# Performance work log

Hardware: AMD Instinct MI355X
Metric: run time of the kernel (lower is better)

The kernel has to match this reference:

```python
import jax, jax.numpy as jnp
import numpy as np

VOCAB = 100000
DIM = 128
B = 262144
NEG = 5

def setup_inputs() -> dict:
    key = jax.random.key(0)
    k1, k2, k3, k4 = jax.random.split(key, 4)
    bound = 0.5 / DIM
    input_emb = jax.random.uniform(k4, (VOCAB, DIM), jnp.float32, -bound, bound)
    # original inits output embeddings to zeros; use small random so scores are nontrivial
    output_emb = jax.random.normal(jax.random.fold_in(key, 7), (VOCAB, DIM), jnp.float32) * 0.01
    target_words = jax.random.randint(k1, (B,), 0, VOCAB)
    context_words = jax.random.randint(k2, (B,), 0, VOCAB)
    negative_words = jax.random.randint(k3, (B, NEG), 0, VOCAB)
    return {"target_words": target_words, "context_words": context_words,
            "negative_words": negative_words, "input_emb": input_emb,
            "output_emb": output_emb}

def reference(target_words, context_words, negative_words, input_emb, output_emb):
    t = input_emb[target_words]               # [B, D]
    c = output_emb[context_words]             # [B, D]
    pos_scores = jnp.einsum('bd,bd->b', t, c) # [B]
    positive_loss = -jnp.mean(jax.nn.log_sigmoid(pos_scores))
    n = output_emb[negative_words]            # [B, NEG, D]
    neg_scores = jnp.einsum('bd,bnd->bn', t, n)  # [B, NEG]
    negative_loss = -jnp.mean(jax.nn.log_sigmoid(-neg_scores))
    return (positive_loss, negative_loss)
```

## Files before the change

kernel.cpp:

```cpp
#include <hip/hip_runtime.h>

#define VOCAB 100000
#define DIM 128
#define BATCH 262144
#define NEG 5

__device__ __forceinline__ float softplus_fast(float x) {
    return fmaxf(x, 0.0f) + __logf(1.0f + __expf(-fabsf(x)));
}

__device__ __forceinline__ float dot4(const float4 a, const float4 b) {
    return a.x * b.x + a.y * b.y + a.z * b.z + a.w * b.w;
}

__global__ void ns_init_kernel(float* acc) {
    acc[0] = 0.0f;
    acc[1] = 0.0f;
}

__global__ __launch_bounds__(256) void ns_loss_kernel(
    const int* __restrict__ tgt,
    const int* __restrict__ ctx,
    const int* __restrict__ negw,
    const float* __restrict__ iemb,
    const float* __restrict__ oemb,
    float* __restrict__ acc)
{
    const int tid = threadIdx.x;
    const int r   = tid & 7;
    const int grp = tid >> 3;
    const int e0  = blockIdx.x * 32 + grp;
    const int estride = gridDim.x * 32;

    float pos_acc = 0.0f, neg_acc = 0.0f;

    for (int e = e0; e < BATCH; e += estride) {
        const int tw = tgt[e];
        const int cw = ctx[e];

        const float4* tp = reinterpret_cast<const float4*>(iemb + (size_t)tw * DIM) + r * 4;
        const float4 t0 = tp[0], t1 = tp[1], t2 = tp[2], t3 = tp[3];

        const float4* cp = reinterpret_cast<const float4*>(oemb + (size_t)cw * DIM) + r * 4;
        float dp = dot4(t0, cp[0]) + dot4(t1, cp[1]) + dot4(t2, cp[2]) + dot4(t3, cp[3]);

        float dn[NEG];
        #pragma unroll
        for (int j = 0; j < NEG; ++j) {
            const int nw = negw[e * NEG + j];
            const float4* np_ = reinterpret_cast<const float4*>(oemb + (size_t)nw * DIM) + r * 4;
            dn[j] = dot4(t0, np_[0]) + dot4(t1, np_[1]) + dot4(t2, np_[2]) + dot4(t3, np_[3]);
        }

        #pragma unroll
        for (int m = 4; m >= 1; m >>= 1) {
            dp += __shfl_xor(dp, m, 64);
            #pragma unroll
            for (int j = 0; j < NEG; ++j) dn[j] += __shfl_xor(dn[j], m, 64);
        }

        pos_acc += softplus_fast(-dp);
        float s = 0.0f;
        #pragma unroll
        for (int j = 0; j < NEG; ++j) s += softplus_fast(dn[j]);
        neg_acc += s;
    }

    __shared__ float sp[256];
    __shared__ float sn[256];
    sp[tid] = pos_acc;
    sn[tid] = neg_acc;
    __syncthreads();
    #pragma unroll
    for (int s = 128; s > 0; s >>= 1) {
        if (tid < s) {
            sp[tid] += sp[tid + s];
            sn[tid] += sn[tid + s];
        }
        __syncthreads();
    }
    if (tid == 0) {
        atomicAdd(&acc[0], sp[0]);
        atomicAdd(&acc[1], sn[0]);
    }
}

__global__ void ns_finalize_kernel(const float* __restrict__ acc, float* __restrict__ out) {
    out[0] = acc[0] * (1.0f / ((float)BATCH * 8.0f));
    out[1] = acc[1] * (1.0f / ((float)BATCH * (float)NEG * 8.0f));
}

extern "C" void kernel_launch(void* const* d_in, const int* in_sizes, int n_in,
                              void* d_out, int out_size, void* d_ws, size_t ws_size,
                              hipStream_t stream) {
    const int*   tgt  = (const int*)d_in[0];
    const int*   ctx  = (const int*)d_in[1];
    const int*   negw = (const int*)d_in[2];
    const float* iemb = (const float*)d_in[3];
    const float* oemb = (const float*)d_in[4];
    float* out = (float*)d_out;
    float* acc = (float*)d_ws;

    ns_init_kernel<<<1, 1, 0, stream>>>(acc);
    ns_loss_kernel<<<2048, 256, 0, stream>>>(tgt, ctx, negw, iemb, oemb, acc);
    ns_finalize_kernel<<<1, 1, 0, stream>>>(acc, out);
}
```

Measured before the change: 151.8 us.

## Double-buffer embedding gathers into LDS with async global_load_lds and prefetched indices

Remaps work so each wave handles two batch elements per step with 32 lanes per row, and gathers all seven embedding rows straight into LDS through async global-to-LDS loads. The LDS buffers are double-buffered and indices are prefetched two iterations ahead, so memory latency overlaps with the dot products. The block-level LDS reduction is replaced by a wave shuffle and per-wave atomics, and the finalize scaling is updated for the 32-lane replication. This adds a dependency on the global_load_lds lane layout and a full vmcnt wait each iteration.

Result: slower. 278.1 us (+83.3%).

```diff
diff --git a/kernel.cpp b/kernel.cpp
--- a/kernel.cpp
+++ b/kernel.cpp
@@ -5,12 +5,26 @@
 #define BATCH 262144
 #define NEG 5
 
+#define NBLOCK 2048
+#define NTHREADS 256
+#define WAVES_PER_BLOCK 4
+#define NWAVES (NBLOCK * WAVES_PER_BLOCK)
+#define NPAIRS (BATCH / 2)
+#define NIT (NPAIRS / NWAVES)
+
 __device__ __forceinline__ float softplus_fast(float x) {
     return fmaxf(x, 0.0f) + __logf(1.0f + __expf(-fabsf(x)));
 }
 
-__device__ __forceinline__ float dot4(const float4 a, const float4 b) {
+__device__ __forceinline__ float dot4(float4 a, float4 b) {
     return a.x * b.x + a.y * b.y + a.z * b.z + a.w * b.w;
+}
+
+__device__ __forceinline__ void async_row16(const float* gsrc, float* ldst) {
+    __builtin_amdgcn_global_load_lds(
+        (const __attribute__((address_space(1))) void*)gsrc,
+        (__attribute__((address_space(3))) void*)ldst,
+        16, 0, 0);
 }
 
 __global__ void ns_init_kernel(float* acc) {
@@ -18,7 +32,7 @@
     acc[1] = 0.0f;
 }
 
-__global__ __launch_bounds__(256) void ns_loss_kernel(
+__global__ __launch_bounds__(NTHREADS) void ns_loss_kernel(
     const int* __restrict__ tgt,
     const int* __restrict__ ctx,
     const int* __restrict__ negw,
@@ -26,34 +40,72 @@
     const float* __restrict__ oemb,
     float* __restrict__ acc)
 {
-    const int tid = threadIdx.x;
-    const int r   = tid & 7;
-    const int grp = tid >> 3;
-    const int e0  = blockIdx.x * 32 + grp;
-    const int estride = gridDim.x * 32;
+    __shared__ __align__(16) float lds[WAVES_PER_BLOCK][2][7][2][128];
+
+    const int tid  = threadIdx.x;
+    const int lane = tid & 63;
+    const int w    = tid >> 6;
+    const int l    = lane & 31;
+    const int h    = lane >> 5;
+    const int W    = blockIdx.x * WAVES_PER_BLOCK + w;
 
     float pos_acc = 0.0f, neg_acc = 0.0f;
 
-    for (int e = e0; e < BATCH; e += estride) {
-        const int tw = tgt[e];
-        const int cw = ctx[e];
+    int ix[7];
 
-        const float4* tp = reinterpret_cast<const float4*>(iemb + (size_t)tw * DIM) + r * 4;
-        const float4 t0 = tp[0], t1 = tp[1], t2 = tp[2], t3 = tp[3];
+    {
+        const int e = (W) * 2 + h;
+        ix[0] = tgt[e];
+        ix[1] = ctx[e];
+        #pragma unroll
+        for (int j = 0; j < NEG; ++j) ix[2 + j] = negw[e * NEG + j];
+    }
+    {
+        float* nbuf = &lds[w][0][0][0][0];
+        async_row16(iemb + (size_t)ix[0] * DIM + l * 4, nbuf + 0 * 256);
+        #pragma unroll
+        for (int k = 1; k < 7; ++k)
+            async_row16(oemb + (size_t)ix[k] * DIM + l * 4, nbuf + k * 256);
+    }
+    {
+        const int e = (W + NWAVES) * 2 + h;
+        ix[0] = tgt[e];
+        ix[1] = ctx[e];
+        #pragma unroll
+        for (int j = 0; j < NEG; ++j) ix[2 + j] = negw[e * NEG + j];
+    }
 
-        const float4* cp = reinterpret_cast<const float4*>(oemb + (size_t)cw * DIM) + r * 4;
-        float dp = dot4(t0, cp[0]) + dot4(t1, cp[1]) + dot4(t2, cp[2]) + dot4(t3, cp[3]);
+    for (int it = 0; it < NIT; ++it) {
+        asm volatile("s_waitcnt vmcnt(0)" ::: "memory");
 
+        if (it + 1 < NIT) {
+            float* nbuf = &lds[w][(it + 1) & 1][0][0][0];
+            async_row16(iemb + (size_t)ix[0] * DIM + l * 4, nbuf + 0 * 256);
+            #pragma unroll
+            for (int k = 1; k < 7; ++k)
+                async_row16(oemb + (size_t)ix[k] * DIM + l * 4, nbuf + k * 256);
+        }
+        if (it + 2 < NIT) {
+            const int e = (W + (it + 2) * NWAVES) * 2 + h;
+            ix[0] = tgt[e];
+            ix[1] = ctx[e];
+            #pragma unroll
+            for (int j = 0; j < NEG; ++j) ix[2 + j] = negw[e * NEG + j];
+        }
+
+        const float* rbase = &lds[w][it & 1][0][h][l * 4];
+        const float4 t4 = *(const float4*)(rbase + 0 * 256);
+        const float4 c4 = *(const float4*)(rbase + 1 * 256);
+        float dp = dot4(t4, c4);
         float dn[NEG];
         #pragma unroll
         for (int j = 0; j < NEG; ++j) {
-            const int nw = negw[e * NEG + j];
-            const float4* np_ = reinterpret_cast<const float4*>(oemb + (size_t)nw * DIM) + r * 4;
-            dn[j] = dot4(t0, np_[0]) + dot4(t1, np_[1]) + dot4(t2, np_[2]) + dot4(t3, np_[3]);
+            const float4 n4 = *(const float4*)(rbase + (2 + j) * 256);
+            dn[j] = dot4(t4, n4);
         }
 
         #pragma unroll
-        for (int m = 4; m >= 1; m >>= 1) {
+        for (int m = 16; m >= 1; m >>= 1) {
             dp += __shfl_xor(dp, m, 64);
             #pragma unroll
             for (int j = 0; j < NEG; ++j) dn[j] += __shfl_xor(dn[j], m, 64);
@@ -66,28 +118,20 @@
         neg_acc += s;
     }
 
-    __shared__ float sp[256];
-    __shared__ float sn[256];
-    sp[tid] = pos_acc;
-    sn[tid] = neg_acc;
-    __syncthreads();
     #pragma unroll
-    for (int s = 128; s > 0; s >>= 1) {
-        if (tid < s) {
-            sp[tid] += sp[tid + s];
-            sn[tid] += sn[tid + s];
-        }
-        __syncthreads();
+    for (int m = 32; m >= 1; m >>= 1) {
+        pos_acc += __shfl_xor(pos_acc, m, 64);
+        neg_acc += __shfl_xor(neg_acc, m, 64);
     }
-    if (tid == 0) {
-        atomicAdd(&acc[0], sp[0]);
-        atomicAdd(&acc[1], sn[0]);
+    if (lane == 0) {
+        atomicAdd(&acc[0], pos_acc);
+        atomicAdd(&acc[1], neg_acc);
     }
 }
 
 __global__ void ns_finalize_kernel(const float* __restrict__ acc, float* __restrict__ out) {
-    out[0] = acc[0] * (1.0f / ((float)BATCH * 8.0f));
-    out[1] = acc[1] * (1.0f / ((float)BATCH * (float)NEG * 8.0f));
+    out[0] = acc[0] * (1.0f / ((float)BATCH * 32.0f));
+    out[1] = acc[1] * (1.0f / ((float)BATCH * (float)NEG * 32.0f));
 }
 
 extern "C" void kernel_launch(void* const* d_in, const int* in_sizes, int n_in,
@@ -102,6 +146,6 @@
     float* acc = (float*)d_ws;
 
     ns_init_kernel<<<1, 1, 0, stream>>>(acc);
-    ns_loss_kernel<<<2048, 256, 0, stream>>>(tgt, ctx, negw, iemb, oemb, acc);
+    ns_loss_kernel<<<NBLOCK, NTHREADS, 0, stream>>>(tgt, ctx, negw, iemb, oemb, acc);
     ns_finalize_kernel<<<1, 1, 0, stream>>>(acc, out);
 }
```

## Convert embedding tables to fp16 per call and gather with fdot2 pipelining

Applied to the files above, without the earlier changes.

On every call, both fp32 embedding tables are converted into fp16 copies in workspace. The loss kernel then gathers 256-byte fp16 rows with 16 lanes per example and computes dot products with packed fdot2. Index loads and row gathers are double-buffered across iterations, and the block reduction uses wave shuffles instead of shared memory. The goal is to halve the bytes moved by the random gathers. The cost is a full table conversion pass on each call, some loss of precision, and dependence on a large enough workspace; otherwise the old fp32 path runs.

After: 266.6 us. 1.76x slower.

```diff
diff --git a/kernel.cpp b/kernel.cpp
--- a/kernel.cpp
+++ b/kernel.cpp
@@ -1,16 +1,41 @@
 #include <hip/hip_runtime.h>
+
+typedef _Float16 f16;
+typedef _Float16 f16x2 __attribute__((ext_vector_type(2)));
+typedef _Float16 f16x4 __attribute__((ext_vector_type(4)));
 
 #define VOCAB 100000
 #define DIM 128
 #define BATCH 262144
 #define NEG 5
 
+#define NBLOCK 2048
+#define NTHREADS 256
+#define GROUPS_PER_BLOCK (NTHREADS / 16)
+#define NGROUPS (NBLOCK * GROUPS_PER_BLOCK)
+#define EPG (BATCH / NGROUPS)
+
+#define TABLE_HALF_BYTES ((size_t)VOCAB * DIM * 2)
+#define WS_NEEDED (256 + 2 * TABLE_HALF_BYTES)
+
 __device__ __forceinline__ float softplus_fast(float x) {
     return fmaxf(x, 0.0f) + __logf(1.0f + __expf(-fabsf(x)));
 }
 
-__device__ __forceinline__ float dot4(const float4 a, const float4 b) {
-    return a.x * b.x + a.y * b.y + a.z * b.z + a.w * b.w;
+__device__ __forceinline__ float fdot2h(f16x2 a, f16x2 b, float c) {
+#if __has_builtin(__builtin_amdgcn_fdot2)
+    return __builtin_amdgcn_fdot2(a, b, c, false);
+#else
+    return c + (float)a[0] * (float)b[0] + (float)a[1] * (float)b[1];
+#endif
+}
+
+__device__ __forceinline__ float dot8h(uint4 a, uint4 b, float s) {
+    union { uint4 u; f16x2 h[4]; } A, B;
+    A.u = a; B.u = b;
+    #pragma unroll
+    for (int i = 0; i < 4; ++i) s = fdot2h(A.h[i], B.h[i], s);
+    return s;
 }
 
 __global__ void ns_init_kernel(float* acc) {
@@ -18,12 +43,120 @@
     acc[1] = 0.0f;
 }
 
-__global__ __launch_bounds__(256) void ns_loss_kernel(
+__global__ __launch_bounds__(256) void ns_convert_kernel(
+    const float* __restrict__ iemb, const float* __restrict__ oemb,
+    f16* __restrict__ iembH, f16* __restrict__ oembH)
+{
+    const int n4 = VOCAB * DIM / 4;
+    int i = blockIdx.x * blockDim.x + threadIdx.x;
+    const int stride = gridDim.x * blockDim.x;
+    for (; i < n4; i += stride) {
+        float4 a = reinterpret_cast<const float4*>(iemb)[i];
+        f16x4 ha = {(f16)a.x, (f16)a.y, (f16)a.z, (f16)a.w};
+        reinterpret_cast<f16x4*>(iembH)[i] = ha;
+        float4 b = reinterpret_cast<const float4*>(oemb)[i];
+        f16x4 hb = {(f16)b.x, (f16)b.y, (f16)b.z, (f16)b.w};
+        reinterpret_cast<f16x4*>(oembH)[i] = hb;
+    }
+}
+
+__global__ __launch_bounds__(NTHREADS) void ns_loss_h_kernel(
     const int* __restrict__ tgt,
     const int* __restrict__ ctx,
     const int* __restrict__ negw,
-    const float* __restrict__ iemb,
-    const float* __restrict__ oemb,
+    const f16* __restrict__ iembH,
+    const f16* __restrict__ oembH,
+    float* __restrict__ acc)
+{
+    const int tid   = threadIdx.x;
+    const int lane  = tid & 63;
+    const int r     = lane & 15;
+    const int group = blockIdx.x * GROUPS_PER_BLOCK + (tid >> 4);
+
+    float pos = 0.0f, neg = 0.0f;
+
+    int ixA[7], ixB[7];
+    uint4 A[7], B[7];
+
+    #define LOAD_IDX(it, ix)                                            \
+        do {                                                            \
+            int e_ = group + (it) * NGROUPS;                            \
+            e_ = (e_ < BATCH) ? e_ : 0;                                 \
+            (ix)[0] = tgt[e_];                                          \
+            (ix)[1] = ctx[e_];                                          \
+            _Pragma("unroll")                                           \
+            for (int j_ = 0; j_ < NEG; ++j_)                            \
+                (ix)[2 + j_] = negw[e_ * NEG + j_];                     \
+        } while (0)
+
+    #define ISSUE_ROWS(ix, buf)                                                         \
+        do {                                                                            \
+            (buf)[0] = reinterpret_cast<const uint4*>(iembH + ((size_t)(ix)[0] << 7))[r]; \
+            _Pragma("unroll")                                                           \
+            for (int k_ = 1; k_ < 7; ++k_)                                              \
+                (buf)[k_] = reinterpret_cast<const uint4*>(oembH + ((size_t)(ix)[k_] << 7))[r]; \
+        } while (0)
+
+    #define COMPUTE_E(buf)                                              \
+        do {                                                            \
+            float dp_ = dot8h((buf)[0], (buf)[1], 0.0f);                \
+            float dn_[NEG];                                             \
+            _Pragma("unroll")                                           \
+            for (int j_ = 0; j_ < NEG; ++j_)                            \
+                dn_[j_] = dot8h((buf)[0], (buf)[2 + j_], 0.0f);         \
+            _Pragma("unroll")                                           \
+            for (int m_ = 8; m_ >= 1; m_ >>= 1) {                       \
+                dp_ += __shfl_xor(dp_, m_, 64);                         \
+                _Pragma("unroll")                                       \
+                for (int j_ = 0; j_ < NEG; ++j_)                        \
+                    dn_[j_] += __shfl_xor(dn_[j_], m_, 64);             \
+            }                                                           \
+            pos += softplus_fast(-dp_);                                 \
+            float s_ = 0.0f;                                            \
+            _Pragma("unroll")                                           \
+            for (int j_ = 0; j_ < NEG; ++j_)                            \
+                s_ += softplus_fast(dn_[j_]);                           \
+            neg += s_;                                                  \
+        } while (0)
+
+    LOAD_IDX(0, ixA);
+    ISSUE_ROWS(ixA, A);
+    LOAD_IDX(1, ixB);
+
+    #pragma unroll
+    for (int it = 0; it < EPG; it += 2) {
+        if (it + 1 < EPG) ISSUE_ROWS(ixB, B);
+        if (it + 2 < EPG) LOAD_IDX(it + 2, ixA);
+        COMPUTE_E(A);
+        if (it + 2 < EPG) ISSUE_ROWS(ixA, A);
+        if (it + 3 < EPG) LOAD_IDX(it + 3, ixB);
+        if (it + 1 < EPG) COMPUTE_E(B);
+    }
+
+    #undef LOAD_IDX
+    #undef ISSUE_ROWS
+    #undef COMPUTE_E
+
+    #pragma unroll
+    for (int m = 32; m >= 1; m >>= 1) {
+        pos += __shfl_xor(pos, m, 64);
+        neg += __shfl_xor(neg, m, 64);
+    }
+    if (lane == 0) {
+        atomicAdd(&acc[0], pos);
+        atomicAdd(&acc[1], neg);
+    }
+}
+
+__global__ void ns_finalize_h_kernel(const float* __restrict__ acc, float* __restrict__ out) {
+    out[0] = acc[0] * (1.0f / ((float)BATCH * 16.0f));
+    out[1] = acc[1] * (1.0f / ((float)BATCH * (float)NEG * 16.0f));
+}
+
+__global__ __launch_bounds__(256) void ns_loss_f32_kernel(
+    const int* __restrict__ tgt, const int* __restrict__ ctx,
+    const int* __restrict__ negw,
+    const float* __restrict__ iemb, const float* __restrict__ oemb,
     float* __restrict__ acc)
 {
     const int tid = threadIdx.x;
@@ -33,59 +166,50 @@
     const int estride = gridDim.x * 32;
 
     float pos_acc = 0.0f, neg_acc = 0.0f;
-
     for (int e = e0; e < BATCH; e += estride) {
         const int tw = tgt[e];
         const int cw = ctx[e];
-
         const float4* tp = reinterpret_cast<const float4*>(iemb + (size_t)tw * DIM) + r * 4;
         const float4 t0 = tp[0], t1 = tp[1], t2 = tp[2], t3 = tp[3];
-
         const float4* cp = reinterpret_cast<const float4*>(oemb + (size_t)cw * DIM) + r * 4;
-        float dp = dot4(t0, cp[0]) + dot4(t1, cp[1]) + dot4(t2, cp[2]) + dot4(t3, cp[3]);
-
+        float dp = t0.x*cp[0].x+t0.y*cp[0].y+t0.z*cp[0].z+t0.w*cp[0].w
+                 + t1.x*cp[1].x+t1.y*cp[1].y+t1.z*cp[1].z+t1.w*cp[1].w
+                 + t2.x*cp[2].x+t2.y*cp[2].y+t2.z*cp[2].z+t2.w*cp[2].w
+                 + t3.x*cp[3].x+t3.y*cp[3].y+t3.z*cp[3].z+t3.w*cp[3].w;
         float dn[NEG];
         #pragma unroll
         for (int j = 0; j < NEG; ++j) {
             const int nw = negw[e * NEG + j];
             const float4* np_ = reinterpret_cast<const float4*>(oemb + (size_t)nw * DIM) + r * 4;
-            dn[j] = dot4(t0, np_[0]) + dot4(t1, np_[1]) + dot4(t2, np_[2]) + dot4(t3, np_[3]);
+            dn[j] = t0.x*np_[0].x+t0.y*np_[0].y+t0.z*np_[0].z+t0.w*np_[0].w
+                  + t1.x*np_[1].x+t1.y*np_[1].y+t1.z*np_[1].z+t1.w*np_[1].w
+                  + t2.x*np_[2].x+t2.y*np_[2].y+t2.z*np_[2].z+t2.w*np_[2].w
+                  + t3.x*np_[3].x+t3.y*np_[3].y+t3.z*np_[3].z+t3.w*np_[3].w;
         }
-
         #pragma unroll
         for (int m = 4; m >= 1; m >>= 1) {
             dp += __shfl_xor(dp, m, 64);
             #pragma unroll
             for (int j = 0; j < NEG; ++j) dn[j] += __shfl_xor(dn[j], m, 64);
         }
-
         pos_acc += softplus_fast(-dp);
         float s = 0.0f;
         #pragma unroll
         for (int j = 0; j < NEG; ++j) s += softplus_fast(dn[j]);
         neg_acc += s;
     }
-
-    __shared__ float sp[256];
-    __shared__ float sn[256];
-    sp[tid] = pos_acc;
-    sn[tid] = neg_acc;
-    __syncthreads();
-    #pragma unroll
-    for (int s = 128; s > 0; s >>= 1) {
-        if (tid < s) {
-            sp[tid] += sp[tid + s];
-            sn[tid] += sn[tid + s];
-        }
-        __syncthreads();
-    }
-    if (tid == 0) {
-        atomicAdd(&acc[0], sp[0]);
-        atomicAdd(&acc[1], sn[0]);
-    }
-}
-
-__global__ void ns_finalize_kernel(const float* __restrict__ acc, float* __restrict__ out) {
+    #pragma unroll
+    for (int m = 32; m >= 1; m >>= 1) {
+        pos_acc += __shfl_xor(pos_acc, m, 64);
+        neg_acc += __shfl_xor(neg_acc, m, 64);
+    }
+    if ((tid & 63) == 0) {
+        atomicAdd(&acc[0], pos_acc);
+        atomicAdd(&acc[1], neg_acc);
+    }
+}
+
+__global__ void ns_finalize_f32_kernel(const float* __restrict__ acc, float* __restrict__ out) {
     out[0] = acc[0] * (1.0f / ((float)BATCH * 8.0f));
     out[1] = acc[1] * (1.0f / ((float)BATCH * (float)NEG * 8.0f));
 }
@@ -101,7 +225,16 @@
     float* out = (float*)d_out;
     float* acc = (float*)d_ws;
 
-    ns_init_kernel<<<1, 1, 0, stream>>>(acc);
-    ns_loss_kernel<<<2048, 256, 0, stream>>>(tgt, ctx, negw, iemb, oemb, acc);
-    ns_finalize_kernel<<<1, 1, 0, stream>>>(acc, out);
-}
+    if (ws_size >= WS_NEEDED) {
+        f16* iembH = (f16*)((char*)d_ws + 256);
+        f16* oembH = (f16*)((char*)d_ws + 256 + TABLE_HALF_BYTES);
+        ns_init_kernel<<<1, 1, 0, stream>>>(acc);
+        ns_convert_kernel<<<2048, 256, 0, stream>>>(iemb, oemb, iembH, oembH);
+        ns_loss_h_kernel<<<NBLOCK, NTHREADS, 0, stream>>>(tgt, ctx, negw, iembH, oembH, acc);
+        ns_finalize_h_kernel<<<1, 1, 0, stream>>>(acc, out);
+    } else {
+        ns_init_kernel<<<1, 1, 0, stream>>>(acc);
+        ns_loss_f32_kernel<<<2048, 256, 0, stream>>>(tgt, ctx, negw, iemb, oemb, acc);
+        ns_finalize_f32_kernel<<<1, 1, 0, stream>>>(acc, out);
+    }
+}
```
